# Kernel tuning notes

Hardware: AMD Instinct MI355X
Metric: run time of the kernel (lower is better)

## Reference

```python
import jax, jax.numpy as jnp
import numpy as np

DIM = 1024
HEADS = 16
HEAD_DIM = DIM // HEADS
B, N = 2, 2048
SCALE = 1.0 / np.float32(np.sqrt(DIM))  # original scales by sqrt(dim), not sqrt(head_dim)


def setup_inputs() -> dict:
    key = jax.random.key(0)
    ks = jax.random.split(key, 9)
    s = 0.02
    return {
        "x": jax.random.normal(ks[0], (B, N, DIM), dtype=jnp.float32),
        "Wq": jax.random.normal(ks[1], (DIM, DIM), dtype=jnp.float32) * s,
        "bq": jax.random.normal(ks[2], (DIM,), dtype=jnp.float32) * s,
        "Wk": jax.random.normal(ks[3], (DIM, DIM), dtype=jnp.float32) * s,
        "bk": jax.random.normal(ks[4], (DIM,), dtype=jnp.float32) * s,
        "Wv": jax.random.normal(ks[5], (DIM, DIM), dtype=jnp.float32) * s,
        "bv": jax.random.normal(ks[6], (DIM,), dtype=jnp.float32) * s,
        "Wo": jax.random.normal(ks[7], (DIM, DIM), dtype=jnp.float32) * s,
        "bo": jax.random.normal(ks[8], (DIM,), dtype=jnp.float32) * s,
    }


def _split_heads(t):
    # torch.stack(torch.split(t, head_dim, -1), dim=0) -> (H, B, N, head_dim)
    b, n, _ = t.shape
    return jnp.moveaxis(t.reshape(b, n, HEADS, HEAD_DIM), 2, 0)


def reference(x, Wq, bq, Wk, bk, Wv, bv, Wo, bo):
    q = _split_heads(x @ Wq.T + bq)  # (H,B,N,d)
    k = _split_heads(x @ Wk.T + bk)
    v = _split_heads(x @ Wv.T + bv)
    # NOTE: original computes K @ Q^T (K rows attend over Q rows), scaled by sqrt(dim)
    scores = jnp.einsum("hbnd,hbmd->hbnm", k, q) * SCALE  # (H,B,N,N)
    attn = jax.nn.softmax(scores, axis=-1)
    out = jnp.einsum("hbnm,hbmd->hbnd", attn, v)  # (H,B,N,d)
    out = jnp.moveaxis(out, 0, 2).reshape(x.shape[0], x.shape[1], DIM)  # (B,N,H*d)
    return out @ Wo.T + bo
```

## Files before the change

### kernel.cpp

```cpp
#include <hip/hip_runtime.h>
#include <hip/hip_bf16.h>
#include <cstdint>
#include <cstddef>

typedef __bf16 bf16_t;
typedef __bf16 bf16x4 __attribute__((ext_vector_type(4)));
typedef __bf16 bf16x8 __attribute__((ext_vector_type(8)));
typedef float  f32x4  __attribute__((ext_vector_type(4)));
typedef float  f32x16 __attribute__((ext_vector_type(16)));
typedef unsigned int u32;
typedef unsigned int u32x4 __attribute__((ext_vector_type(4)));

#define DIM_   1024
#define HEADS_ 16
#define HD_    64
#define BB_    2
#define NN_    2048
#define MTOT   (BB_*NN_)
static constexpr float SCALE_ = 0.03125f;
static constexpr float EXPC_  = 0.045084220027780106f;

__device__ __forceinline__ float exp2_hw(float x) {
    float r;
    asm("v_exp_f32 %0, %1" : "=v"(r) : "v"(x));
    return r;
}

__global__ __launch_bounds__(256) void cvt_all(
    const float* __restrict__ X,
    const float* __restrict__ W0, const float* __restrict__ W1,
    const float* __restrict__ W2, const float* __restrict__ W3,
    bf16_t* __restrict__ xo,
    bf16_t* __restrict__ o0, bf16_t* __restrict__ o1,
    bf16_t* __restrict__ o2, bf16_t* __restrict__ o3)
{
    const int bid = blockIdx.x;
    const float* src;
    bf16_t* dst;
    int lb;
    if (bid < 2048) { src = X; dst = xo; lb = bid; }
    else {
        const int w = (bid - 2048) >> 9;
        lb = (bid - 2048) & 511;
        src = (w == 0) ? W0 : (w == 1) ? W1 : (w == 2) ? W2 : W3;
        dst = (w == 0) ? o0 : (w == 1) ? o1 : (w == 2) ? o2 : o3;
    }
    const size_t i = ((size_t)lb * 256 + threadIdx.x) * 8;
    f32x4 a = *(const f32x4*)(src + i);
    f32x4 b = *(const f32x4*)(src + i + 4);
    bf16x8 o;
    o[0] = (bf16_t)a.x; o[1] = (bf16_t)a.y; o[2] = (bf16_t)a.z; o[3] = (bf16_t)a.w;
    o[4] = (bf16_t)b.x; o[5] = (bf16_t)b.y; o[6] = (bf16_t)b.z; o[7] = (bf16_t)b.w;
    *(bf16x8*)(dst + i) = o;
}

__device__ __forceinline__ void gld16(const bf16_t* g, bf16_t* l) {
    __builtin_amdgcn_global_load_lds(
        (const __attribute__((address_space(1))) unsigned int*)g,
        (__attribute__((address_space(3))) unsigned int*)l, 16, 0, 0);
}

__global__ __launch_bounds__(512) void gemm_qkv(
    const bf16_t* __restrict__ A,
    const bf16_t* __restrict__ Wq, const bf16_t* __restrict__ Wk, const bf16_t* __restrict__ Wv,
    const float* __restrict__ bq, const float* __restrict__ bk, const float* __restrict__ bv,
    bf16_t* __restrict__ Cq, bf16_t* __restrict__ Ck, bf16_t* __restrict__ Vt)
{
    __shared__ __align__(16) bf16_t As[2][128 * 64];
    __shared__ __align__(16) bf16_t Bs[2][3 * 64 * 64];

    const int tid  = threadIdx.x;
    const int lane = tid & 63;
    const int w    = tid >> 6;
    const int wr   = w >> 1;
    const int wc   = w & 1;
    const int bn   = blockIdx.x;
    const int bm   = blockIdx.y;

    const int l15 = lane & 15;
    const int g   = lane >> 4;
    const int sw  = l15 & 7;

    const int srow = lane >> 3;
    const int scol = ((lane & 7) ^ srow) * 8;

    const bf16_t* aSrc0 = A  + (size_t)(bm * 128 + (w * 2 + 0) * 8 + srow) * DIM_ + scol;
    const bf16_t* aSrc1 = A  + (size_t)(bm * 128 + (w * 2 + 1) * 8 + srow) * DIM_ + scol;
    const bf16_t* qSrc  = Wq + (size_t)(bn * 64 + w * 8 + srow) * DIM_ + scol;
    const bf16_t* kSrc  = Wk + (size_t)(bn * 64 + w * 8 + srow) * DIM_ + scol;
    const bf16_t* vSrc  = Wv + (size_t)(bn * 64 + w * 8 + srow) * DIM_ + scol;

    f32x4 aq[2][2], ak[2][2], av[2][2];
    #pragma unroll
    for (int i = 0; i < 2; i++)
        #pragma unroll
        for (int j = 0; j < 2; j++) {
            aq[i][j] = (f32x4){0.f, 0.f, 0.f, 0.f};
            ak[i][j] = (f32x4){0.f, 0.f, 0.f, 0.f};
            av[i][j] = (f32x4){0.f, 0.f, 0.f, 0.f};
        }

    #define QSTAGE(buf, kb)                                       \
        {                                                         \
            gld16(aSrc0 + (kb), &As[buf][(w * 2 + 0) * 512]);     \
            gld16(aSrc1 + (kb), &As[buf][(w * 2 + 1) * 512]);     \
            gld16(qSrc + (kb), &Bs[buf][w * 512]);                \
            gld16(kSrc + (kb), &Bs[buf][4096 + w * 512]);         \
            gld16(vSrc + (kb), &Bs[buf][8192 + w * 512]);         \
        }

    QSTAGE(0, 0);
    __syncthreads();

    for (int t = 0; t < 16; t++) {
        const int cur = t & 1;
        if (t < 15) QSTAGE(cur ^ 1, (t + 1) * 64);

        #pragma unroll
        for (int kk = 0; kk < 2; kk++) {
            const int swc = ((kk * 4 + g) ^ sw) * 8;
            bf16x8 af[2];
            #pragma unroll
            for (int i = 0; i < 2; i++)
                af[i] = *(const bf16x8*)&As[cur][(wr * 32 + i * 16 + l15) * 64 + swc];
            bf16x8 bqf[2], bkf[2], bvf[2];
            #pragma unroll
            for (int j = 0; j < 2; j++) {
                const int off = (wc * 32 + j * 16 + l15) * 64 + swc;
                bqf[j] = *(const bf16x8*)&Bs[cur][off];
                bkf[j] = *(const bf16x8*)&Bs[cur][4096 + off];
                bvf[j] = *(const bf16x8*)&Bs[cur][8192 + off];
            }
            #pragma unroll
            for (int i = 0; i < 2; i++)
                #pragma unroll
                for (int j = 0; j < 2; j++) {
                    aq[i][j] = __builtin_amdgcn_mfma_f32_16x16x32_bf16(af[i], bqf[j], aq[i][j], 0, 0, 0);
                    ak[i][j] = __builtin_amdgcn_mfma_f32_16x16x32_bf16(af[i], bkf[j], ak[i][j], 0, 0, 0);
                    av[i][j] = __builtin_amdgcn_mfma_f32_16x16x32_bf16(af[i], bvf[j], av[i][j], 0, 0, 0);
                }
        }

        __syncthreads();
    }
    #undef QSTAGE

    bf16_t* Ts = (bf16_t*)As;
    const int r4 = g * 4;
    #pragma unroll
    for (int j = 0; j < 2; j++) {
        const int lc = wc * 32 + j * 16 + l15;
        const int gc = bn * 64 + lc;
        const float vq = bq[gc], vk = bk[gc], vv = bv[gc];
        #pragma unroll
        for (int i = 0; i < 2; i++) {
            #pragma unroll
            for (int r = 0; r < 4; r++) {
                const int lm = wr * 32 + i * 16 + r4 + r;
                const size_t gr = (size_t)(bm * 128 + lm) * DIM_ + gc;
                Cq[gr] = (bf16_t)((aq[i][j][r] + vq) * EXPC_);
                Ck[gr] = (bf16_t)(ak[i][j][r] + vk);
                Ts[lc * 136 + lm] = (bf16_t)(av[i][j][r] + vv);
            }
        }
    }
    __syncthreads();
    {
        const int b  = bm >> 4;
        const int m0 = (bm & 15) * 128;
        const int d  = tid >> 3;
        const int c  = (tid & 7) * 16;
        bf16x8 v0 = *(const bf16x8*)&Ts[d * 136 + c];
        bf16x8 v1 = *(const bf16x8*)&Ts[d * 136 + c + 8];
        bf16_t* dst = Vt + ((size_t)(b * HEADS_ + bn) * HD_ + d) * NN_ + m0 + c;
        *(bf16x8*)dst       = v0;
        *(bf16x8*)(dst + 8) = v1;
    }
}

__global__ __launch_bounds__(512) void gemm_o(
    const bf16_t* __restrict__ A, const bf16_t* __restrict__ Wo,
    const float* __restrict__ bo, float* __restrict__ C)
{
    __shared__ __align__(16) bf16_t As[2][64 * 64];
    __shared__ __align__(16) bf16_t Bs[2][128 * 64];

    const int tid  = threadIdx.x;
    const int lane = tid & 63;
    const int w    = tid >> 6;
    const int wr   = w & 1;
    const int wc   = w >> 1;
    const int bn   = blockIdx.x;
    const int bm   = blockIdx.y;

    const int l15 = lane & 15;
    const int g   = lane >> 4;
    const int sw  = l15 & 7;

    const int srow = lane >> 3;
    const int scol = ((lane & 7) ^ srow) * 8;

    const bf16_t* aSrc  = A  + (size_t)(bm * 64 + w * 8 + srow) * DIM_ + scol;
    const bf16_t* b0Src = Wo + (size_t)(bn * 128 + (w * 2 + 0) * 8 + srow) * DIM_ + scol;
    const bf16_t* b1Src = Wo + (size_t)(bn * 128 + (w * 2 + 1) * 8 + srow) * DIM_ + scol;

    f32x4 acc[2][2];
    #pragma unroll
    for (int i = 0; i < 2; i++)
        #pragma unroll
        for (int j = 0; j < 2; j++)
            acc[i][j] = (f32x4){0.f, 0.f, 0.f, 0.f};

    #define OSTAGE(buf, kb)                                          \
        {                                                            \
            gld16(aSrc + (kb), &As[buf][w * 512]);                   \
            gld16(b0Src + (kb), &Bs[buf][(w * 2 + 0) * 512]);        \
            gld16(b1Src + (kb), &Bs[buf][(w * 2 + 1) * 512]);        \
        }

    OSTAGE(0, 0);
    __syncthreads();

    for (int t = 0; t < 16; t++) {
        const int cur = t & 1;
        if (t < 15) OSTAGE(cur ^ 1, (t + 1) * 64);

        #pragma unroll
        for (int kk = 0; kk < 2; kk++) {
            const int swc = ((kk * 4 + g) ^ sw) * 8;
            bf16x8 af[2], bf[2];
            #pragma unroll
            for (int i = 0; i < 2; i++)
                af[i] = *(const bf16x8*)&As[cur][(wr * 32 + i * 16 + l15) * 64 + swc];
            #pragma unroll
            for (int j = 0; j < 2; j++)
                bf[j] = *(const bf16x8*)&Bs[cur][(wc * 32 + j * 16 + l15) * 64 + swc];
            #pragma unroll
            for (int i = 0; i < 2; i++)
                #pragma unroll
                for (int j = 0; j < 2; j++)
                    acc[i][j] = __builtin_amdgcn_mfma_f32_16x16x32_bf16(af[i], bf[j], acc[i][j], 0, 0, 0);
        }

        __syncthreads();
    }
    #undef OSTAGE

    const int r4 = g * 4;
    #pragma unroll
    for (int j = 0; j < 2; j++) {
        const int gc = bn * 128 + wc * 32 + j * 16 + l15;
        const float bv = bo[gc];
        #pragma unroll
        for (int i = 0; i < 2; i++) {
            #pragma unroll
            for (int r = 0; r < 4; r++) {
                const size_t gr = (size_t)(bm * 64 + wr * 32 + i * 16 + r4 + r) * DIM_ + gc;
                C[gr] = acc[i][j][r] + bv;
            }
        }
    }
}

__device__ __forceinline__ u32 cvtpk_bf16(float lo, float hi) {
    u32 d;
    asm volatile("v_cvt_pk_bf16_f32 %0, %1, %2" : "=v"(d) : "v"(lo), "v"(hi));
    return d;
}

__global__ __launch_bounds__(512, 4) void attn_mfma9(
    const bf16_t* __restrict__ Qa,
    const bf16_t* __restrict__ Ka,
    const bf16_t* __restrict__ Vtg,
    bf16_t* __restrict__ O)
{
    __shared__ __align__(16) bf16_t Kt[2][128 * 72];
    __shared__ __align__(16) bf16_t Vt[2][64 * 136];

    const int tid  = threadIdx.x;
    const int lane = tid & 63;
    const int w    = tid >> 6;
    const int l31  = lane & 31;
    const int h5   = lane >> 5;

    const int nw = (w & 3) * 32;
    const int mo = (w >> 2) * 64;

    const int wg = blockIdx.x;
    const int id = (wg & 7) * 64 + (wg >> 3);
    const int bh = id >> 4;
    const int nt = id & 15;
    const int b  = bh >> 4, h = bh & 15;
    const int n0 = nt * 128;

    const size_t base = (size_t)b * NN_ * DIM_ + h * HD_;

    const bf16_t* qrow = Qa + base + (size_t)(n0 + nw + l31) * DIM_ + h5 * 8;
    bf16x8 qf[4];
    #pragma unroll
    for (int ks = 0; ks < 4; ks++)
        qf[ks] = *(const bf16x8*)(qrow + ks * 16);

    f32x16 oa0 = {}, oa1 = {};
    float Lp = 0.f;

    const bf16_t* vrow   = Vtg + (size_t)bh * HD_ * NN_;
    const bf16_t* kgbase = Ka + base;

    const int kr2 = tid >> 3;
    const int kc2 = (tid & 7) * 8;
    const int vc2 = (tid & 7) * 16;

    bf16x8 kA0, kB0, vA0, vA1;

    #define ISSUE(m0)                                                                        \
        {                                                                                    \
            kA0 = *(const bf16x8*)(kgbase + (size_t)((m0) + kr2) * DIM_ + kc2);              \
            kB0 = *(const bf16x8*)(kgbase + (size_t)((m0) + 64 + kr2) * DIM_ + kc2);         \
            const bf16x8* vp = (const bf16x8*)(vrow + (size_t)kr2 * NN_ + (m0) + vc2);       \
            vA0 = vp[0]; vA1 = vp[1];                                                        \
        }
    #define COMMIT(buf)                                                                      \
        {                                                                                    \
            *(bf16x8*)(Kt[buf] + kr2 * 72 + kc2)        = kA0;                               \
            *(bf16x8*)(Kt[buf] + (64 + kr2) * 72 + kc2) = kB0;                               \
            bf16_t* vd = Vt[buf] + kr2 * 136 + vc2;                                          \
            *(bf16x8*)(vd)     = vA0;                                                        \
            *(bf16x8*)(vd + 8) = vA1;                                                        \
        }

    ISSUE(0);
    COMMIT(0);
    __syncthreads();

    for (int mt = 0; mt < NN_ / 128; mt++) {
        const int cur = mt & 1;
        if (mt < NN_ / 128 - 1) ISSUE((mt + 1) * 128);

        const bf16_t* KtC = Kt[cur];
        const bf16_t* VtC = Vt[cur];

        f32x16 sa0 = {}, sa1 = {};
        __builtin_amdgcn_s_setprio(1);
        #pragma unroll
        for (int ks = 0; ks < 4; ks++) {
            bf16x8 kf0 = *(const bf16x8*)&KtC[(mo + l31) * 72 + ks * 16 + h5 * 8];
            bf16x8 kf1 = *(const bf16x8*)&KtC[(mo + 32 + l31) * 72 + ks * 16 + h5 * 8];
            sa0 = __builtin_amdgcn_mfma_f32_32x32x16_bf16(kf0, qf[ks], sa0, 0, 0, 0);
            sa1 = __builtin_amdgcn_mfma_f32_32x32x16_bf16(kf1, qf[ks], sa1, 0, 0, 0);
        }
        __builtin_amdgcn_s_setprio(0);

        float p0[16], p1[16];
        #pragma unroll
        for (int r = 0; r < 16; r++) { p0[r] = exp2_hw(sa0[r]); p1[r] = exp2_hw(sa1[r]); }
        {
            float s0 = (p0[0] + p0[1]) + (p0[2] + p0[3]);
            float s1 = (p0[4] + p0[5]) + (p0[6] + p0[7]);
            float s2 = (p0[8] + p0[9]) + (p0[10] + p0[11]);
            float s3 = (p0[12] + p0[13]) + (p0[14] + p0[15]);
            float t0 = (p1[0] + p1[1]) + (p1[2] + p1[3]);
            float t1 = (p1[4] + p1[5]) + (p1[6] + p1[7]);
            float t2 = (p1[8] + p1[9]) + (p1[10] + p1[11]);
            float t3 = (p1[12] + p1[13]) + (p1[14] + p1[15]);
            Lp += ((s0 + s1) + (s2 + s3)) + ((t0 + t1) + (t2 + t3));
        }

        bf16x8 pf[4];
        #pragma unroll
        for (int mb = 0; mb < 4; mb++) {
            const float* pp = (mb & 2) ? p1 : p0;
            const int rb = (mb & 1) * 8;
            u32 x0 = cvtpk_bf16(pp[rb + 0], pp[rb + 1]);
            u32 x1 = cvtpk_bf16(pp[rb + 2], pp[rb + 3]);
            u32 y0 = cvtpk_bf16(pp[rb + 4], pp[rb + 5]);
            u32 y1 = cvtpk_bf16(pp[rb + 6], pp[rb + 7]);
            asm volatile("v_permlane32_swap_b32 %0, %1" : "+v"(x0), "+v"(y0));
            asm volatile("v_permlane32_swap_b32 %0, %1" : "+v"(x1), "+v"(y1));
            u32x4 t; t.x = x0; t.y = x1; t.z = y0; t.w = y1;
            pf[mb] = __builtin_bit_cast(bf16x8, t);
        }

        __builtin_amdgcn_s_setprio(1);
        #pragma unroll
        for (int ms = 0; ms < 4; ms++) {
            bf16x8 vf0 = *(const bf16x8*)&VtC[l31 * 136 + mo + ms * 16 + h5 * 8];
            bf16x8 vf1 = *(const bf16x8*)&VtC[(32 + l31) * 136 + mo + ms * 16 + h5 * 8];
            oa0 = __builtin_amdgcn_mfma_f32_32x32x16_bf16(pf[ms], vf0, oa0, 0, 0, 0);
            oa1 = __builtin_amdgcn_mfma_f32_32x32x16_bf16(pf[ms], vf1, oa1, 0, 0, 0);
        }
        __builtin_amdgcn_s_setprio(0);

        if (mt < NN_ / 128 - 1) COMMIT(cur ^ 1);
        __syncthreads();
    }
    #undef ISSUE
    #undef COMMIT

    Lp += __shfl_xor(Lp, 32);

    float* scratch0 = (float*)Kt;
    float* scratch1 = (float*)Vt;
    if (w >= 4) {
        float* buf = (w < 6) ? (scratch0 + (w - 4) * 2112)
                             : (scratch1 + (w - 6) * 2112);
        #pragma unroll
        for (int reg = 0; reg < 16; reg++) {
            buf[reg * 64 + lane]        = oa0[reg];
            buf[1024 + reg * 64 + lane] = oa1[reg];
        }
        buf[2048 + lane] = Lp;
    }
    __syncthreads();
    if (w < 4) {
        const float* buf = (w < 2) ? (scratch0 + w * 2112)
                                   : (scratch1 + (w - 2) * 2112);
        #pragma unroll
        for (int reg = 0; reg < 16; reg++) {
            oa0[reg] += buf[reg * 64 + lane];
            oa1[reg] += buf[1024 + reg * 64 + lane];
        }
        Lp += buf[2048 + lane];
    }
    __syncthreads();

    float* Lsh = scratch0 + 4224;
    if (w < 4) Lsh[nw + l31] = Lp;
    __syncthreads();

    if (w < 4) {
        #pragma unroll
        for (int reg = 0; reg < 16; reg++) {
            const int nr = (reg & 3) + 8 * (reg >> 2) + 4 * h5;
            const float il = 1.f / Lsh[nw + nr];
            const size_t rowoff = base + (size_t)(n0 + nw + nr) * DIM_;
            O[rowoff + l31]      = (bf16_t)(oa0[reg] * il);
            O[rowoff + 32 + l31] = (bf16_t)(oa1[reg] * il);
        }
    }
}

extern "C" void kernel_launch(void* const* d_in, const int* in_sizes, int n_in,
                              void* d_out, int out_size, void* d_ws, size_t ws_size,
                              hipStream_t stream)
{
    const float* x  = (const float*)d_in[0];
    const float* Wq = (const float*)d_in[1];
    const float* bq = (const float*)d_in[2];
    const float* Wk = (const float*)d_in[3];
    const float* bk = (const float*)d_in[4];
    const float* Wv = (const float*)d_in[5];
    const float* bv = (const float*)d_in[6];
    const float* Wo = (const float*)d_in[7];
    const float* bo = (const float*)d_in[8];
    float* out = (float*)d_out;

    const size_t SEG = (size_t)MTOT * DIM_;
    bf16_t* xb = (bf16_t*)d_ws;
    bf16_t* qb = xb + SEG;
    bf16_t* kb = qb + SEG;
    bf16_t* vt = kb + SEG;
    bf16_t* ab = xb;

    bf16_t* wqb = vt + SEG;
    bf16_t* wkb = wqb + (size_t)DIM_ * DIM_;
    bf16_t* wvb = wkb + (size_t)DIM_ * DIM_;
    bf16_t* wob = wvb + (size_t)DIM_ * DIM_;

    cvt_all<<<dim3(4096), 256, 0, stream>>>(x, Wq, Wk, Wv, Wo, xb, wqb, wkb, wvb, wob);

    gemm_qkv<<<dim3(16, 32), 512, 0, stream>>>(
        xb, wqb, wkb, wvb, bq, bk, bv, qb, kb, vt);

    attn_mfma9<<<dim3(512), 512, 0, stream>>>(kb, qb, vt, ab);

    gemm_o<<<dim3(8, 64), 512, 0, stream>>>(ab, wob, bo, out);
}
```

Before: 102.0 us.

## Split attention key range in two halves with separate merge kernel

The attention kernel now splits the key/value sequence into two halves. Each block handles one half over 64-row tiles with smaller shared buffers, and the grid doubles to 1024 blocks. Unnormalized partial outputs and row sums go to scratch space (d_out and the freed Wq buffer), and a new merge kernel adds the halves and normalizes. This is meant to raise parallelism and occupancy across CUs, at the cost of an extra kernel launch, extra global traffic for the partials, and more barriers per tile.

```diff
diff --git a/kernel.cpp b/kernel.cpp
--- a/kernel.cpp
+++ b/kernel.cpp
@@ -268,14 +268,14 @@
     return d;
 }
 
-__global__ __launch_bounds__(512, 4) void attn_mfma9(
+__global__ __launch_bounds__(512, 4) void attn_mfma12(
     const bf16_t* __restrict__ Qa,
     const bf16_t* __restrict__ Ka,
     const bf16_t* __restrict__ Vtg,
-    bf16_t* __restrict__ O)
+    bf16_t* __restrict__ Pbase,
+    float* __restrict__ Lbuf)
 {
-    __shared__ __align__(16) bf16_t Kt[2][128 * 72];
-    __shared__ __align__(16) bf16_t Vt[2][64 * 136];
+    __shared__ __align__(16) bf16_t S[4][64 * 72];
 
     const int tid  = threadIdx.x;
     const int lane = tid & 63;
@@ -284,14 +284,17 @@
     const int h5   = lane >> 5;
 
     const int nw = (w & 3) * 32;
-    const int mo = (w >> 2) * 64;
-
-    const int wg = blockIdx.x;
-    const int id = (wg & 7) * 64 + (wg >> 3);
-    const int bh = id >> 4;
-    const int nt = id & 15;
-    const int b  = bh >> 4, h = bh & 15;
-    const int n0 = nt * 128;
+    const int mo = (w >> 2) * 32;
+
+    const int wg  = blockIdx.x;
+    const int id  = (wg & 7) * 128 + (wg >> 3);
+    const int mh  = id & 1;
+    const int id2 = id >> 1;
+    const int bh  = id2 >> 4;
+    const int nt  = id2 & 15;
+    const int b   = bh >> 4, h = bh & 15;
+    const int n0  = nt * 128;
+    const int mbase = mh * (NN_ / 2);
 
     const size_t base = (size_t)b * NN_ * DIM_ + h * HD_;
 
@@ -307,137 +310,165 @@
     const bf16_t* vrow   = Vtg + (size_t)bh * HD_ * NN_;
     const bf16_t* kgbase = Ka + base;
 
-    const int kr2 = tid >> 3;
-    const int kc2 = (tid & 7) * 8;
-    const int vc2 = (tid & 7) * 16;
-
-    bf16x8 kA0, kB0, vA0, vA1;
-
-    #define ISSUE(m0)                                                                        \
-        {                                                                                    \
-            kA0 = *(const bf16x8*)(kgbase + (size_t)((m0) + kr2) * DIM_ + kc2);              \
-            kB0 = *(const bf16x8*)(kgbase + (size_t)((m0) + 64 + kr2) * DIM_ + kc2);         \
-            const bf16x8* vp = (const bf16x8*)(vrow + (size_t)kr2 * NN_ + (m0) + vc2);       \
-            vA0 = vp[0]; vA1 = vp[1];                                                        \
-        }
-    #define COMMIT(buf)                                                                      \
-        {                                                                                    \
-            *(bf16x8*)(Kt[buf] + kr2 * 72 + kc2)        = kA0;                               \
-            *(bf16x8*)(Kt[buf] + (64 + kr2) * 72 + kc2) = kB0;                               \
-            bf16_t* vd = Vt[buf] + kr2 * 136 + vc2;                                          \
-            *(bf16x8*)(vd)     = vA0;                                                        \
-            *(bf16x8*)(vd + 8) = vA1;                                                        \
-        }
-
-    ISSUE(0);
+    const int sr3 = tid >> 3;
+    const int sc3 = (tid & 7) * 8;
+
+    bf16x8 kA0, vA0;
+
+    #define ISSUE(m0v)                                                              \
+        {                                                                           \
+            kA0 = *(const bf16x8*)(kgbase + (size_t)((m0v) + sr3) * DIM_ + sc3);    \
+            vA0 = *(const bf16x8*)(vrow + (size_t)sr3 * NN_ + (m0v) + sc3);         \
+        }
+    #define COMMIT(buf)                                                             \
+        {                                                                           \
+            *(bf16x8*)(S[buf] + sr3 * 72 + sc3)     = kA0;                          \
+            *(bf16x8*)(S[2 + buf] + sr3 * 72 + sc3) = vA0;                          \
+        }
+
+    ISSUE(mbase);
     COMMIT(0);
     __syncthreads();
 
-    for (int mt = 0; mt < NN_ / 128; mt++) {
-        const int cur = mt & 1;
-        if (mt < NN_ / 128 - 1) ISSUE((mt + 1) * 128);
-
-        const bf16_t* KtC = Kt[cur];
-        const bf16_t* VtC = Vt[cur];
-
-        f32x16 sa0 = {}, sa1 = {};
+    for (int t = 0; t < 16; t++) {
+        const int cur = t & 1;
+        if (t < 15) ISSUE(mbase + (t + 1) * 64);
+
+        const bf16_t* KtC = S[cur];
+        const bf16_t* VsC = S[2 + cur];
+
+        f32x16 sa = {};
         __builtin_amdgcn_s_setprio(1);
         #pragma unroll
         for (int ks = 0; ks < 4; ks++) {
-            bf16x8 kf0 = *(const bf16x8*)&KtC[(mo + l31) * 72 + ks * 16 + h5 * 8];
-            bf16x8 kf1 = *(const bf16x8*)&KtC[(mo + 32 + l31) * 72 + ks * 16 + h5 * 8];
-            sa0 = __builtin_amdgcn_mfma_f32_32x32x16_bf16(kf0, qf[ks], sa0, 0, 0, 0);
-            sa1 = __builtin_amdgcn_mfma_f32_32x32x16_bf16(kf1, qf[ks], sa1, 0, 0, 0);
+            bf16x8 kf = *(const bf16x8*)&KtC[(mo + l31) * 72 + ks * 16 + h5 * 8];
+            sa = __builtin_amdgcn_mfma_f32_32x32x16_bf16(kf, qf[ks], sa, 0, 0, 0);
         }
         __builtin_amdgcn_s_setprio(0);
 
-        float p0[16], p1[16];
-        #pragma unroll
-        for (int r = 0; r < 16; r++) { p0[r] = exp2_hw(sa0[r]); p1[r] = exp2_hw(sa1[r]); }
+        float p[16];
+        #pragma unroll
+        for (int r = 0; r < 16; r++) p[r] = exp2_hw(sa[r]);
         {
-            float s0 = (p0[0] + p0[1]) + (p0[2] + p0[3]);
-            float s1 = (p0[4] + p0[5]) + (p0[6] + p0[7]);
-            float s2 = (p0[8] + p0[9]) + (p0[10] + p0[11]);
-            float s3 = (p0[12] + p0[13]) + (p0[14] + p0[15]);
-            float t0 = (p1[0] + p1[1]) + (p1[2] + p1[3]);
-            float t1 = (p1[4] + p1[5]) + (p1[6] + p1[7]);
-            float t2 = (p1[8] + p1[9]) + (p1[10] + p1[11]);
-            float t3 = (p1[12] + p1[13]) + (p1[14] + p1[15]);
-            Lp += ((s0 + s1) + (s2 + s3)) + ((t0 + t1) + (t2 + t3));
-        }
-
-        bf16x8 pf[4];
-        #pragma unroll
-        for (int mb = 0; mb < 4; mb++) {
-            const float* pp = (mb & 2) ? p1 : p0;
-            const int rb = (mb & 1) * 8;
-            u32 x0 = cvtpk_bf16(pp[rb + 0], pp[rb + 1]);
-            u32 x1 = cvtpk_bf16(pp[rb + 2], pp[rb + 3]);
-            u32 y0 = cvtpk_bf16(pp[rb + 4], pp[rb + 5]);
-            u32 y1 = cvtpk_bf16(pp[rb + 6], pp[rb + 7]);
+            float s0 = (p[0] + p[1]) + (p[2] + p[3]);
+            float s1 = (p[4] + p[5]) + (p[6] + p[7]);
+            float s2 = (p[8] + p[9]) + (p[10] + p[11]);
+            float s3 = (p[12] + p[13]) + (p[14] + p[15]);
+            Lp += (s0 + s1) + (s2 + s3);
+        }
+
+        bf16x8 pf[2];
+        #pragma unroll
+        for (int mb = 0; mb < 2; mb++) {
+            const int rb = mb * 8;
+            u32 x0 = cvtpk_bf16(p[rb + 0], p[rb + 1]);
+            u32 x1 = cvtpk_bf16(p[rb + 2], p[rb + 3]);
+            u32 y0 = cvtpk_bf16(p[rb + 4], p[rb + 5]);
+            u32 y1 = cvtpk_bf16(p[rb + 6], p[rb + 7]);
             asm volatile("v_permlane32_swap_b32 %0, %1" : "+v"(x0), "+v"(y0));
             asm volatile("v_permlane32_swap_b32 %0, %1" : "+v"(x1), "+v"(y1));
-            u32x4 t; t.x = x0; t.y = x1; t.z = y0; t.w = y1;
-            pf[mb] = __builtin_bit_cast(bf16x8, t);
+            u32x4 tt; tt.x = x0; tt.y = x1; tt.z = y0; tt.w = y1;
+            pf[mb] = __builtin_bit_cast(bf16x8, tt);
         }
 
         __builtin_amdgcn_s_setprio(1);
         #pragma unroll
-        for (int ms = 0; ms < 4; ms++) {
-            bf16x8 vf0 = *(const bf16x8*)&VtC[l31 * 136 + mo + ms * 16 + h5 * 8];
-            bf16x8 vf1 = *(const bf16x8*)&VtC[(32 + l31) * 136 + mo + ms * 16 + h5 * 8];
+        for (int ms = 0; ms < 2; ms++) {
+            bf16x8 vf0 = *(const bf16x8*)&VsC[l31 * 72 + mo + ms * 16 + h5 * 8];
+            bf16x8 vf1 = *(const bf16x8*)&VsC[(32 + l31) * 72 + mo + ms * 16 + h5 * 8];
             oa0 = __builtin_amdgcn_mfma_f32_32x32x16_bf16(pf[ms], vf0, oa0, 0, 0, 0);
             oa1 = __builtin_amdgcn_mfma_f32_32x32x16_bf16(pf[ms], vf1, oa1, 0, 0, 0);
         }
         __builtin_amdgcn_s_setprio(0);
 
-        if (mt < NN_ / 128 - 1) COMMIT(cur ^ 1);
         __syncthreads();
+        if (t < 15) {
+            COMMIT(cur ^ 1);
+            __syncthreads();
+        }
     }
     #undef ISSUE
     #undef COMMIT
 
     Lp += __shfl_xor(Lp, 32);
 
-    float* scratch0 = (float*)Kt;
-    float* scratch1 = (float*)Vt;
-    if (w >= 4) {
-        float* buf = (w < 6) ? (scratch0 + (w - 4) * 2112)
-                             : (scratch1 + (w - 6) * 2112);
-        #pragma unroll
-        for (int reg = 0; reg < 16; reg++) {
-            buf[reg * 64 + lane]        = oa0[reg];
-            buf[1024 + reg * 64 + lane] = oa1[reg];
-        }
-        buf[2048 + lane] = Lp;
-    }
-    __syncthreads();
+    float* scratch = (float*)S;
+    {
+        if (w >= 4 && w < 7) {
+            float* buf = scratch + (w - 4) * 2112;
+            #pragma unroll
+            for (int reg = 0; reg < 16; reg++) {
+                buf[reg * 64 + lane]        = oa0[reg];
+                buf[1024 + reg * 64 + lane] = oa1[reg];
+            }
+            buf[2048 + lane] = Lp;
+        }
+        __syncthreads();
+        if (w < 3) {
+            const float* buf = scratch + w * 2112;
+            #pragma unroll
+            for (int reg = 0; reg < 16; reg++) {
+                oa0[reg] += buf[reg * 64 + lane];
+                oa1[reg] += buf[1024 + reg * 64 + lane];
+            }
+            Lp += buf[2048 + lane];
+        }
+        __syncthreads();
+        if (w == 7) {
+            float* buf = scratch;
+            #pragma unroll
+            for (int reg = 0; reg < 16; reg++) {
+                buf[reg * 64 + lane]        = oa0[reg];
+                buf[1024 + reg * 64 + lane] = oa1[reg];
+            }
+            buf[2048 + lane] = Lp;
+        }
+        __syncthreads();
+        if (w == 3) {
+            const float* buf = scratch;
+            #pragma unroll
+            for (int reg = 0; reg < 16; reg++) {
+                oa0[reg] += buf[reg * 64 + lane];
+                oa1[reg] += buf[1024 + reg * 64 + lane];
+            }
+            Lp += buf[2048 + lane];
+        }
+    }
+
     if (w < 4) {
-        const float* buf = (w < 2) ? (scratch0 + w * 2112)
-                                   : (scratch1 + (w - 2) * 2112);
-        #pragma unroll
-        for (int reg = 0; reg < 16; reg++) {
-            oa0[reg] += buf[reg * 64 + lane];
-            oa1[reg] += buf[1024 + reg * 64 + lane];
-        }
-        Lp += buf[2048 + lane];
-    }
-    __syncthreads();
-
-    float* Lsh = scratch0 + 4224;
-    if (w < 4) Lsh[nw + l31] = Lp;
-    __syncthreads();
-
-    if (w < 4) {
+        bf16_t* Pp = Pbase + (size_t)mh * ((size_t)MTOT * DIM_);
+        if (h5 == 0)
+            Lbuf[mh * 65536 + bh * 2048 + n0 + nw + l31] = Lp;
         #pragma unroll
         for (int reg = 0; reg < 16; reg++) {
             const int nr = (reg & 3) + 8 * (reg >> 2) + 4 * h5;
-            const float il = 1.f / Lsh[nw + nr];
             const size_t rowoff = base + (size_t)(n0 + nw + nr) * DIM_;
-            O[rowoff + l31]      = (bf16_t)(oa0[reg] * il);
-            O[rowoff + 32 + l31] = (bf16_t)(oa1[reg] * il);
-        }
-    }
+            Pp[rowoff + l31]      = (bf16_t)oa0[reg];
+            Pp[rowoff + 32 + l31] = (bf16_t)oa1[reg];
+        }
+    }
+}
+
+__global__ __launch_bounds__(256) void merge_o(
+    const bf16_t* __restrict__ P0, const bf16_t* __restrict__ P1,
+    const float* __restrict__ L0, const float* __restrict__ L1,
+    bf16_t* __restrict__ out)
+{
+    const size_t i = ((size_t)blockIdx.x * 256 + threadIdx.x) * 8;
+    const int col = (int)(i & 1023);
+    const int row = (int)(i >> 10);
+    const int n   = row & 2047;
+    const int b   = row >> 11;
+    const int bh  = b * HEADS_ + (col >> 6);
+    const float L = L0[bh * 2048 + n] + L1[bh * 2048 + n];
+    const float inv = 1.f / L;
+    bf16x8 a = *(const bf16x8*)(P0 + i);
+    bf16x8 c = *(const bf16x8*)(P1 + i);
+    bf16x8 o;
+    #pragma unroll
+    for (int j = 0; j < 8; j++)
+        o[j] = (bf16_t)(((float)a[j] + (float)c[j]) * inv);
+    *(bf16x8*)(out + i) = o;
 }
 
 extern "C" void kernel_launch(void* const* d_in, const int* in_sizes, int n_in,
@@ -467,12 +498,18 @@
     bf16_t* wvb = wkb + (size_t)DIM_ * DIM_;
     bf16_t* wob = wvb + (size_t)DIM_ * DIM_;
 
+    bf16_t* Pbase = (bf16_t*)d_out;
+    float*  Lbuf  = (float*)wqb;
+
     cvt_all<<<dim3(4096), 256, 0, stream>>>(x, Wq, Wk, Wv, Wo, xb, wqb, wkb, wvb, wob);
 
     gemm_qkv<<<dim3(16, 32), 512, 0, stream>>>(
         xb, wqb, wkb, wvb, bq, bk, bv, qb, kb, vt);
 
-    attn_mfma9<<<dim3(512), 512, 0, stream>>>(kb, qb, vt, ab);
+    attn_mfma12<<<dim3(1024), 512, 0, stream>>>(kb, qb, vt, Pbase, Lbuf);
+
+    merge_o<<<dim3(2048), 256, 0, stream>>>(
+        Pbase, Pbase + SEG, Lbuf, Lbuf + 65536, ab);
 
     gemm_o<<<dim3(8, 64), 512, 0, stream>>>(ab, wob, bo, out);
 }
```

New measurement: 110.0 us. 1.08x slower.
